# Kernel optimization log

Measured on AMD Instinct MI355X. Metric: run time of the kernel, lower is better.

Reference implementation:

```python
import jax, jax.numpy as jnp
import numpy as np
import math

D = 2048      # hidden_size
H = 16        # num_heads
DH = 128      # head_dim
RQ = 1024     # q_rank
RK = 512      # kv_rank
B, T = 2, 2048

def setup_inputs() -> dict:
    key = jax.random.key(0)
    ks = jax.random.split(key, 8)
    s = lambda fan_in: 1.0 / math.sqrt(fan_in)
    return {
        "x": jax.random.normal(ks[0], (B, T, D), dtype=jnp.float32),
        "Wq_down": jax.random.normal(ks[1], (RQ, D), dtype=jnp.float32) * s(D),
        "Wkv_down": jax.random.normal(ks[2], (RK, D), dtype=jnp.float32) * s(D),
        "Wq_up": jax.random.normal(ks[3], (D, RQ), dtype=jnp.float32) * s(RQ),
        "Wk_up": jax.random.normal(ks[4], (D, RK), dtype=jnp.float32) * s(RK),
        "Wv_up": jax.random.normal(ks[5], (D, RK), dtype=jnp.float32) * s(RK),
        "Wo": jax.random.normal(ks[6], (D, D), dtype=jnp.float32) * s(D),
        "bo": jnp.zeros((D,), dtype=jnp.float32),
    }

def _heads_view(w, rank):
    # w: [H*DH, rank] -> [H, rank, DH]  (matches torch view(H,DH,r).transpose(1,2))
    return w.reshape(H, DH, rank).transpose(0, 2, 1)

def reference(x, Wq_down, Wkv_down, Wq_up, Wk_up, Wv_up, Wo, bo):
    Bx, Tx, d = x.shape
    # low-rank down-projections (torch Linear: x @ W.T)
    Q_lat = x @ Wq_down.T            # [B,T,RQ]
    C_kv = x @ Wkv_down.T            # [B,S,RK]  (S == T, no cache)
    S = C_kv.shape[1]
    # absorbed score matrix M = Uq Uk^T / sqrt(d_h): [H,RQ,RK]
    Uq_h = _heads_view(Wq_up, RQ)    # [H,RQ,DH]
    Uk_h = _heads_view(Wk_up, RK)    # [H,RK,DH]
    Mmat = jnp.einsum('hqd,hkd->hqk', Uq_h, Uk_h) * (1.0 / math.sqrt(DH))
    # logits in latent space: [B,H,T,S]
    logits = jnp.einsum('btq,hqk,bsk->bhts', Q_lat, Mmat, C_kv)
    # causal mask (P = S - T = 0)
    P = S - Tx
    i = jnp.arange(Tx)[:, None]
    j = jnp.arange(S)[None, :]
    neg_inf = jnp.float32(-jnp.inf)
    logits = jnp.where((j > P + i)[None, None], neg_inf, logits)
    # fp32 softmax (every causal row has >=1 valid key, no NaNs)
    attn = jax.nn.softmax(logits.astype(jnp.float32), axis=-1).astype(x.dtype)
    # value up-projection per head: [B,H,S,DH]
    Uv_h = _heads_view(Wv_up, RK)    # [H,RK,DH]
    V_up = jnp.einsum('bsr,hrd->bhsd', C_kv, Uv_h)
    ctx = jnp.einsum('bhts,bhsd->bhtd', attn, V_up)      # [B,H,T,DH]
    ctx = ctx.transpose(0, 2, 1, 3).reshape(Bx, Tx, H * DH)
    out = ctx @ Wo.T + bo
    return out
```

## Files before the change

kernel.cpp:

```cpp
#include <hip/hip_runtime.h>

typedef __bf16 bf16x8 __attribute__((ext_vector_type(8)));
typedef float f32x4 __attribute__((ext_vector_type(4)));
typedef float f32x16 __attribute__((ext_vector_type(16)));
typedef unsigned short u16x4 __attribute__((ext_vector_type(4)));
typedef unsigned int u32x4 __attribute__((ext_vector_type(4)));

#define L2E 1.44269504088896340736f

__device__ __forceinline__ f32x4 mfma16(bf16x8 a, bf16x8 b, f32x4 c) {
  return __builtin_amdgcn_mfma_f32_16x16x32_bf16(a, b, c, 0, 0, 0);
}
__device__ __forceinline__ f32x16 mfma32(bf16x8 a, bf16x8 b, f32x16 c) {
  return __builtin_amdgcn_mfma_f32_32x32x16_bf16(a, b, c, 0, 0, 0);
}

__device__ __forceinline__ void async16(const __bf16* g, __bf16* l) {
  __builtin_amdgcn_global_load_lds(
      (const __attribute__((address_space(1))) void*)g,
      (__attribute__((address_space(3))) void*)l, 16, 0, 0);
}

__device__ __forceinline__ unsigned pk(float x, float y) {
  unsigned short lo = __builtin_bit_cast(unsigned short, (__bf16)x);
  unsigned short hi = __builtin_bit_cast(unsigned short, (__bf16)y);
  return ((unsigned)hi << 16) | (unsigned)lo;
}

__global__ __launch_bounds__(256) void cvt_bf16(const float* __restrict__ s,
                                                __bf16* __restrict__ d) {
  long i = (long)(blockIdx.x * 256 + threadIdx.x) * 4;
  f32x4 v = *(const f32x4*)(s + i);
  u16x4 o;
#pragma unroll
  for (int j = 0; j < 4; j++) o[j] = __builtin_bit_cast(unsigned short, (__bf16)v[j]);
  *(u16x4*)((unsigned short*)d + i) = o;
}

__global__ __launch_bounds__(256) void cvt_w(
    const float* __restrict__ wqd, const float* __restrict__ wkvd,
    const float* __restrict__ wqup, const float* __restrict__ wkup,
    const float* __restrict__ wvup, __bf16* __restrict__ dqkv,
    __bf16* __restrict__ dqu, __bf16* __restrict__ dku,
    __bf16* __restrict__ dvu) {
  int bx = blockIdx.x;
  const float* s;
  __bf16* d;
  int off;
  if (bx < 2048)      { s = wqd;  d = dqkv;                off = bx; }
  else if (bx < 3072) { s = wkvd; d = dqkv + 1024 * 2048;  off = bx - 2048; }
  else if (bx < 5120) { s = wqup; d = dqu;                 off = bx - 3072; }
  else if (bx < 6144) { s = wkup; d = dku;                 off = bx - 5120; }
  else                { s = wvup; d = dvu;                 off = bx - 6144; }
  long i = (long)off * 1024 + threadIdx.x * 4;
  f32x4 v = *(const f32x4*)(s + i);
  u16x4 o;
#pragma unroll
  for (int j = 0; j < 4; j++) o[j] = __builtin_bit_cast(unsigned short, (__bf16)v[j]);
  *(u16x4*)((unsigned short*)d + i) = o;
}

template <int OUTF32>
__device__ __forceinline__ void gemm_body(
    __bf16* As, __bf16* Bs, const __bf16* __restrict__ A,
    const __bf16* __restrict__ Bt, void* __restrict__ Cout,
    const float* __restrict__ bias, int lda, int ldb, int ldc, int N, int K,
    float scale, int bx, int by, int permn) {
  const int tid = threadIdx.x;
  const int wid = tid >> 6, lane = tid & 63;
  const int lrow = lane & 15, lkhi = lane >> 4;
  const int row0 = bx * 128, col0 = by * 128;
  const int wr = (wid >> 1) * 64, wc = (wid & 1) * 64;

  const int trow = tid >> 2;
  const int scol = 8 * ((tid & 3) ^ (trow & 3));
  const __bf16* pA0 = A + (size_t)(row0 + trow) * lda + scol;
  const __bf16* pA1 = pA0 + (size_t)64 * lda;
  const __bf16* pB0 = Bt + (size_t)(col0 + trow) * ldb + scol;
  const __bf16* pB1 = pB0 + (size_t)64 * ldb;
  __bf16* lA0 = As + wid * 512;
  __bf16* lA1 = As + 2048 + wid * 512;
  __bf16* lB0 = Bs + wid * 512;
  __bf16* lB1 = Bs + 2048 + wid * 512;

  int aoff[4], boff[4];
#pragma unroll
  for (int i = 0; i < 4; i++) {
    int rr = wr + i * 16 + lrow;
    aoff[i] = rr * 32 + 8 * (lkhi ^ (rr & 3));
    rr = wc + i * 16 + lrow;
    boff[i] = rr * 32 + 8 * (lkhi ^ (rr & 3));
  }

  f32x4 acc[4][4] = {};
  for (int k0 = 0; k0 < K; k0 += 32) {
    __syncthreads();
    async16(pA0, lA0);
    async16(pA1, lA1);
    async16(pB0, lB0);
    async16(pB1, lB1);
    pA0 += 32; pA1 += 32; pB0 += 32; pB1 += 32;
    __syncthreads();
    bf16x8 af[4], bv[4];
#pragma unroll
    for (int mi = 0; mi < 4; mi++) af[mi] = *(const bf16x8*)(As + aoff[mi]);
#pragma unroll
    for (int ni = 0; ni < 4; ni++) bv[ni] = *(const bf16x8*)(Bs + boff[ni]);
#pragma unroll
    for (int mi = 0; mi < 4; mi++)
#pragma unroll
      for (int ni = 0; ni < 4; ni++)
        acc[mi][ni] = mfma16(af[mi], bv[ni], acc[mi][ni]);
  }

  const int orow = row0 + wr + lkhi * 4;
  const int prow = permn ? ((lrow & 3) | ((lrow & 4) << 1) | ((lrow & 8) >> 1))
                         : lrow;
  const int ocol = col0 + wc + prow;
#pragma unroll
  for (int mi = 0; mi < 4; mi++)
#pragma unroll
    for (int ni = 0; ni < 4; ni++)
#pragma unroll
      for (int r = 0; r < 4; r++) {
        size_t idx = (size_t)(orow + mi * 16 + r) * ldc + (ocol + ni * 16);
        float v = acc[mi][ni][r] * scale;
        if (OUTF32)
          ((float*)Cout)[idx] = v + bias[ocol + ni * 16];
        else
          ((__bf16*)Cout)[idx] = (__bf16)v;
      }
}

template <int OUTF32, int PERMN = 0>
__global__ __launch_bounds__(256, 3) void gemm_bt(
    const __bf16* __restrict__ A, const __bf16* __restrict__ Bt,
    void* __restrict__ Cout, const float* __restrict__ bias,
    int lda, int ldb, int ldc, int N, int K, float scale) {
  __shared__ __align__(16) __bf16 As[4096];
  __shared__ __align__(16) __bf16 Bs[4096];
  gemm_body<OUTF32>(As, Bs, A, Bt, Cout, bias, lda, ldb, ldc, N, K, scale,
                    blockIdx.x, blockIdx.y, PERMN);
}

__global__ __launch_bounds__(256, 3) void gemm_mid(
    const __bf16* __restrict__ qlat, const __bf16* __restrict__ ckv,
    const __bf16* __restrict__ wqu, const __bf16* __restrict__ wku,
    const __bf16* __restrict__ wvu, __bf16* __restrict__ qf,
    __bf16* __restrict__ kf, __bf16* __restrict__ vt) {
  __shared__ __align__(16) __bf16 As[4096];
  __shared__ __align__(16) __bf16 Bs[4096];
  int bid = (int)blockIdx.x;
  if (bid < 512) {
    gemm_body<0>(As, Bs, qlat, wqu, qf, nullptr, 1536, 1024, 2048, 2048, 1024,
                 0.12752039360437355f, bid & 31, bid >> 5, 0);
  } else if (bid < 1024) {
    bid -= 512;
    gemm_body<0>(As, Bs, ckv, wku, kf, nullptr, 1536, 512, 2048, 2048, 512,
                 1.0f, bid & 31, bid >> 5, 0);
  } else {
    bid -= 1024;
    gemm_body<0>(As, Bs, wvu, ckv, vt, nullptr, 512, 1536, 4096, 4096, 512,
                 1.0f, bid & 15, bid >> 4, 1);
  }
}

__global__ __launch_bounds__(256, 2) void mla_attn(
    const __bf16* __restrict__ Qf, const __bf16* __restrict__ Kf,
    const __bf16* __restrict__ Vt, __bf16* __restrict__ ctx) {
  __shared__ __align__(16) __bf16 Ks[2][64 * 128];
  __shared__ __align__(16) __bf16 Vs[2][128 * 64];

  const int r_ = (int)blockIdx.x;
  const int qt = (r_ < 256) ? (15 - (r_ >> 5)) : ((r_ - 256) >> 5);
  const int bh = r_ & 31;
  const int h = bh >> 1, b = bh & 1;
  const int tid = threadIdx.x, wid = tid >> 6, lane = tid & 63;
  const int l31 = lane & 31;
  const bool hh = (lane & 32) != 0;

  const __bf16* Kbh = Kf + (size_t)b * 2048 * 2048 + h * 128;
  const __bf16* Vbh = Vt + (size_t)h * 128 * 4096 + b * 2048;

  auto stage = [&](int k0, int buf) {
#pragma unroll
    for (int i = 0; i < 4; i++) {
      int e = i * 2048 + tid * 8;
      int krow = e >> 7;
      int kcol = (e & 127) ^ (8 * (krow & 15));
      async16(Kbh + (size_t)(k0 + krow) * 2048 + kcol,
              &Ks[buf][i * 2048 + wid * 512]);
    }
#pragma unroll
    for (int i = 0; i < 4; i++) {
      int e = i * 2048 + tid * 8;
      int vrow = e >> 6;
      int vcol = (e & 63) ^ (8 * (vrow & 7));
      async16(Vbh + (size_t)vrow * 4096 + k0 + vcol,
              &Vs[buf][i * 2048 + wid * 512]);
    }
  };

  const int q0 = qt * 128;
  const int nkv = 2 * qt + 2;
  const int q = q0 + wid * 32 + l31;

  bf16x8 qb[8];
  const __bf16* qrow =
      Qf + (size_t)(b * 2048 + q) * 2048 + h * 128 + (hh ? 8 : 0);
#pragma unroll
  for (int ds = 0; ds < 8; ds++) qb[ds] = *(const bf16x8*)(qrow + ds * 16);

  f32x16 o[4] = {};
  float mrow = -1e30f, lsum = 0.f;

  int cur = 0;
  stage(0, 0);

  for (int kb = 0; kb < nkv; kb++) {
    const int k0 = kb * 64;
    __syncthreads();
    if (kb + 1 < nkv) stage(k0 + 64, cur ^ 1);

    f32x16 sa[2] = {}, sb[2] = {};
    __builtin_amdgcn_s_setprio(1);
#pragma unroll
    for (int ds = 0; ds < 4; ds++) {
#pragma unroll
      for (int kt = 0; kt < 2; kt++) {
        int row = kt * 32 + l31;
        int col = (ds * 16 + (hh ? 8 : 0)) ^ (8 * (row & 15));
        bf16x8 kfr = *(const bf16x8*)(&Ks[cur][row * 128 + col]);
        sa[kt] = mfma32(kfr, qb[ds], sa[kt]);
      }
    }
#pragma unroll
    for (int ds = 4; ds < 8; ds++) {
#pragma unroll
      for (int kt = 0; kt < 2; kt++) {
        int row = kt * 32 + l31;
        int col = (ds * 16 + (hh ? 8 : 0)) ^ (8 * (row & 15));
        bf16x8 kfr = *(const bf16x8*)(&Ks[cur][row * 128 + col]);
        sb[kt] = mfma32(kfr, qb[ds], sb[kt]);
      }
    }
    __builtin_amdgcn_s_setprio(0);
    f32x16 sacc[2];
    sacc[0] = sa[0] + sb[0];
    sacc[1] = sa[1] + sb[1];

    if (kb >= 2 * qt) {
#pragma unroll
      for (int kt = 0; kt < 2; kt++)
#pragma unroll
        for (int r = 0; r < 16; r++) {
          int key = k0 + kt * 32 + (r & 3) + 8 * (r >> 2) + (hh ? 4 : 0);
          if (key > q) sacc[kt][r] = -1e30f;
        }
    }

    float t[16];
#pragma unroll
    for (int r = 0; r < 16; r++) t[r] = fmaxf(sacc[0][r], sacc[1][r]);
#pragma unroll
    for (int s = 8; s; s >>= 1)
#pragma unroll
      for (int r = 0; r < s; r++) t[r] = fmaxf(t[r], t[r + s]);
    float pm = fmaxf(t[0], __shfl_xor(t[0], 32));

    if (__any(pm > mrow + 8.f)) {
      float mn = fmaxf(mrow, pm);
      float sf = __builtin_amdgcn_exp2f(mrow - mn);
      mrow = mn;
      lsum *= sf;
#pragma unroll
      for (int r = 0; r < 16; r++) {
        int ql = (r & 3) + 8 * (r >> 2) + (hh ? 4 : 0);
        float sr = __shfl(sf, ql);
#pragma unroll
        for (int dt = 0; dt < 4; dt++) o[dt][r] *= sr;
      }
    }
    float ps0 = 0.f, ps1 = 0.f, ps2 = 0.f, ps3 = 0.f;
#pragma unroll
    for (int kt = 0; kt < 2; kt++)
#pragma unroll
      for (int r = 0; r < 16; r += 4) {
        float a0 = __builtin_amdgcn_exp2f(sacc[kt][r + 0] - mrow);
        float a1 = __builtin_amdgcn_exp2f(sacc[kt][r + 1] - mrow);
        float a2 = __builtin_amdgcn_exp2f(sacc[kt][r + 2] - mrow);
        float a3 = __builtin_amdgcn_exp2f(sacc[kt][r + 3] - mrow);
        sacc[kt][r + 0] = a0; sacc[kt][r + 1] = a1;
        sacc[kt][r + 2] = a2; sacc[kt][r + 3] = a3;
        ps0 += a0; ps1 += a1; ps2 += a2; ps3 += a3;
      }
    float ps = (ps0 + ps1) + (ps2 + ps3);
    ps += __shfl_xor(ps, 32);
    lsum += ps;

    __builtin_amdgcn_s_setprio(1);
#pragma unroll
    for (int s = 0; s < 4; s++) {
      const int kt = s >> 1, r8 = (s & 1) * 8;
      u32x4 wv;
      wv.x = pk(sacc[kt][r8 + 0], sacc[kt][r8 + 1]);
      wv.y = pk(sacc[kt][r8 + 2], sacc[kt][r8 + 3]);
      wv.z = pk(sacc[kt][r8 + 4], sacc[kt][r8 + 5]);
      wv.w = pk(sacc[kt][r8 + 6], sacc[kt][r8 + 7]);
      bf16x8 pa = __builtin_bit_cast(bf16x8, wv);
#pragma unroll
      for (int dt = 0; dt < 4; dt++) {
        int vrow = dt * 32 + l31;
        int vcol = (s * 16 + (hh ? 8 : 0)) ^ (8 * (vrow & 7));
        bf16x8 vf = *(const bf16x8*)(&Vs[cur][vrow * 64 + vcol]);
        o[dt] = mfma32(pa, vf, o[dt]);
      }
    }
    __builtin_amdgcn_s_setprio(0);
    cur ^= 1;
  }

  float inv = 1.f / lsum;
#pragma unroll
  for (int r = 0; r < 16; r++) {
    int ql = (r & 3) + 8 * (r >> 2) + (hh ? 4 : 0);
    float ir = __shfl(inv, ql);
    size_t rowi = (size_t)(b * 2048 + q0 + wid * 32 + ql) * 2048 + h * 128;
#pragma unroll
    for (int dt = 0; dt < 4; dt++)
      ctx[rowi + dt * 32 + l31] = (__bf16)(o[dt][r] * ir);
  }
}

extern "C" void kernel_launch(void* const* d_in, const int* in_sizes, int n_in,
                              void* d_out, int out_size, void* d_ws, size_t ws_size,
                              hipStream_t stream) {
  (void)in_sizes; (void)n_in; (void)out_size; (void)ws_size;
  const float* x    = (const float*)d_in[0];
  const float* wqd  = (const float*)d_in[1];
  const float* wkvd = (const float*)d_in[2];
  const float* wqup = (const float*)d_in[3];
  const float* wkup = (const float*)d_in[4];
  const float* wvup = (const float*)d_in[5];
  const float* wo   = (const float*)d_in[6];
  const float* bo   = (const float*)d_in[7];

  char* ws = (char*)d_ws;
  const size_t MB = 1024 * 1024;
  __bf16* x_bf     = (__bf16*)(ws + 0);
  __bf16* q_full   = (__bf16*)(ws + 16 * MB);
  __bf16* k_full   = (__bf16*)(ws + 32 * MB);
  __bf16* vt       = (__bf16*)(ws + 48 * MB);
  __bf16* qkv_lat  = (__bf16*)(ws + 64 * MB);
  __bf16* wqkvd_bf = (__bf16*)(ws + 76 * MB);
  __bf16* wqup_bf  = (__bf16*)(ws + 82 * MB);
  __bf16* wkup_bf  = (__bf16*)(ws + 86 * MB);
  __bf16* wvup_bf  = (__bf16*)(ws + 88 * MB);
  __bf16* ctx   = x_bf;
  __bf16* wo_bf = qkv_lat;

  cvt_bf16<<<8192, 256, 0, stream>>>(x, x_bf);
  cvt_w<<<7168, 256, 0, stream>>>(wqd, wkvd, wqup, wkup, wvup, wqkvd_bf,
                                  wqup_bf, wkup_bf, wvup_bf);

  dim3 blk(256);
  gemm_bt<0><<<dim3(32, 12), blk, 0, stream>>>(x_bf, wqkvd_bf, qkv_lat, nullptr,
                                               2048, 2048, 1536, 1536, 2048, 1.0f);
  gemm_mid<<<1536, blk, 0, stream>>>(qkv_lat, qkv_lat + 1024, wqup_bf, wkup_bf,
                                     wvup_bf, q_full, k_full, vt);
  cvt_bf16<<<4096, 256, 0, stream>>>(wo, wo_bf);
  mla_attn<<<512, blk, 0, stream>>>(q_full, k_full, vt, ctx);
  gemm_bt<1><<<dim3(32, 16), blk, 0, stream>>>(ctx, wo_bf, (float*)d_out, bo,
                                               2048, 2048, 2048, 2048, 2048, 1.0f);
}
```

Baseline: 226.7 us.

## Split causal KV range across two half-blocks in attention and merge in LDS

The attention kernel now launches 512-thread blocks. Each block splits its query tile's causal key range into two halves, and each half of 256 threads runs its own double-buffered online softmax over its share of the tiles. At the end, the second half writes its partial output and row max/sum to shared memory, and the first half rescales and combines both before writing ctx. This halves the serial per-block loop length to improve load balance across the triangular workload. In exchange, each block uses about 128KB of LDS, which allows only one block per CU, and it adds a merge step with extra syncs.

Measured after the change: 222.0 us. -2.1%, faster.

```diff
diff --git a/kernel.cpp b/kernel.cpp
--- a/kernel.cpp
+++ b/kernel.cpp
@@ -165,45 +165,53 @@
   }
 }
 
-__global__ __launch_bounds__(256, 2) void mla_attn(
+__global__ __launch_bounds__(512, 1) void mla_attn(
     const __bf16* __restrict__ Qf, const __bf16* __restrict__ Kf,
     const __bf16* __restrict__ Vt, __bf16* __restrict__ ctx) {
-  __shared__ __align__(16) __bf16 Ks[2][64 * 128];
-  __shared__ __align__(16) __bf16 Vs[2][128 * 64];
-
-  const int r_ = (int)blockIdx.x;
-  const int qt = (r_ < 256) ? (15 - (r_ >> 5)) : ((r_ - 256) >> 5);
-  const int bh = r_ & 31;
+  __shared__ __align__(16) __bf16 SM[2][32768];
+  __shared__ float MLm[128], MLl[128];
+
+  const int bid = (int)blockIdx.x;
+  const int qt = 15 - (bid >> 5);
+  const int bh = bid & 31;
   const int h = bh >> 1, b = bh & 1;
-  const int tid = threadIdx.x, wid = tid >> 6, lane = tid & 63;
+  const int tid = threadIdx.x;
+  const int half = tid >> 8;
+  const int htid = tid & 255;
+  const int wid4 = htid >> 6;
+  const int lane = tid & 63;
   const int l31 = lane & 31;
   const bool hh = (lane & 32) != 0;
 
+  __bf16* Ks = &SM[half][0];
+  __bf16* Vs = &SM[half][16384];
+
   const __bf16* Kbh = Kf + (size_t)b * 2048 * 2048 + h * 128;
   const __bf16* Vbh = Vt + (size_t)h * 128 * 4096 + b * 2048;
 
   auto stage = [&](int k0, int buf) {
 #pragma unroll
     for (int i = 0; i < 4; i++) {
-      int e = i * 2048 + tid * 8;
+      int e = i * 2048 + htid * 8;
       int krow = e >> 7;
       int kcol = (e & 127) ^ (8 * (krow & 15));
       async16(Kbh + (size_t)(k0 + krow) * 2048 + kcol,
-              &Ks[buf][i * 2048 + wid * 512]);
+              Ks + buf * 8192 + i * 2048 + wid4 * 512);
     }
 #pragma unroll
     for (int i = 0; i < 4; i++) {
-      int e = i * 2048 + tid * 8;
+      int e = i * 2048 + htid * 8;
       int vrow = e >> 6;
       int vcol = (e & 63) ^ (8 * (vrow & 7));
       async16(Vbh + (size_t)vrow * 4096 + k0 + vcol,
-              &Vs[buf][i * 2048 + wid * 512]);
+              Vs + buf * 8192 + i * 2048 + wid4 * 512);
     }
   };
 
   const int q0 = qt * 128;
-  const int nkv = 2 * qt + 2;
-  const int q = q0 + wid * 32 + l31;
+  const int ntile = qt + 1;
+  const int kbase = half * ntile;
+  const int q = q0 + wid4 * 32 + l31;
 
   bf16x8 qb[8];
   const __bf16* qrow =
@@ -215,12 +223,13 @@
   float mrow = -1e30f, lsum = 0.f;
 
   int cur = 0;
-  stage(0, 0);
-
-  for (int kb = 0; kb < nkv; kb++) {
+  stage(kbase * 64, 0);
+
+  for (int t = 0; t < ntile; t++) {
+    const int kb = kbase + t;
     const int k0 = kb * 64;
     __syncthreads();
-    if (kb + 1 < nkv) stage(k0 + 64, cur ^ 1);
+    if (t + 1 < ntile) stage(k0 + 64, cur ^ 1);
 
     f32x16 sa[2] = {}, sb[2] = {};
     __builtin_amdgcn_s_setprio(1);
@@ -230,7 +239,7 @@
       for (int kt = 0; kt < 2; kt++) {
         int row = kt * 32 + l31;
         int col = (ds * 16 + (hh ? 8 : 0)) ^ (8 * (row & 15));
-        bf16x8 kfr = *(const bf16x8*)(&Ks[cur][row * 128 + col]);
+        bf16x8 kfr = *(const bf16x8*)(Ks + cur * 8192 + row * 128 + col);
         sa[kt] = mfma32(kfr, qb[ds], sa[kt]);
       }
     }
@@ -240,7 +249,7 @@
       for (int kt = 0; kt < 2; kt++) {
         int row = kt * 32 + l31;
         int col = (ds * 16 + (hh ? 8 : 0)) ^ (8 * (row & 15));
-        bf16x8 kfr = *(const bf16x8*)(&Ks[cur][row * 128 + col]);
+        bf16x8 kfr = *(const bf16x8*)(Ks + cur * 8192 + row * 128 + col);
         sb[kt] = mfma32(kfr, qb[ds], sb[kt]);
       }
     }
@@ -259,14 +268,14 @@
         }
     }
 
-    float t[16];
-#pragma unroll
-    for (int r = 0; r < 16; r++) t[r] = fmaxf(sacc[0][r], sacc[1][r]);
+    float t16[16];
+#pragma unroll
+    for (int r = 0; r < 16; r++) t16[r] = fmaxf(sacc[0][r], sacc[1][r]);
 #pragma unroll
     for (int s = 8; s; s >>= 1)
 #pragma unroll
-      for (int r = 0; r < s; r++) t[r] = fmaxf(t[r], t[r + s]);
-    float pm = fmaxf(t[0], __shfl_xor(t[0], 32));
+      for (int r = 0; r < s; r++) t16[r] = fmaxf(t16[r], t16[r + s]);
+    float pm = fmaxf(t16[0], __shfl_xor(t16[0], 32));
 
     if (__any(pm > mrow + 8.f)) {
       float mn = fmaxf(mrow, pm);
@@ -312,7 +321,7 @@
       for (int dt = 0; dt < 4; dt++) {
         int vrow = dt * 32 + l31;
         int vcol = (s * 16 + (hh ? 8 : 0)) ^ (8 * (vrow & 7));
-        bf16x8 vf = *(const bf16x8*)(&Vs[cur][vrow * 64 + vcol]);
+        bf16x8 vf = *(const bf16x8*)(Vs + cur * 8192 + vrow * 64 + vcol);
         o[dt] = mfma32(pa, vf, o[dt]);
       }
     }
@@ -320,15 +329,37 @@
     cur ^= 1;
   }
 
-  float inv = 1.f / lsum;
-#pragma unroll
-  for (int r = 0; r < 16; r++) {
-    int ql = (r & 3) + 8 * (r >> 2) + (hh ? 4 : 0);
-    float ir = __shfl(inv, ql);
-    size_t rowi = (size_t)(b * 2048 + q0 + wid * 32 + ql) * 2048 + h * 128;
-#pragma unroll
-    for (int dt = 0; dt < 4; dt++)
-      ctx[rowi + dt * 32 + l31] = (__bf16)(o[dt][r] * ir);
+  __syncthreads();
+  float* om = (float*)&SM[1][0];
+  if (half == 1) {
+#pragma unroll
+    for (int dt = 0; dt < 4; dt++) {
+      int base = ((wid4 * 4 + dt) * 64 + lane) * 16;
+#pragma unroll
+      for (int r = 0; r < 16; r++) om[base + r] = o[dt][r];
+    }
+    if (!hh) { MLm[wid4 * 32 + l31] = mrow; MLl[wid4 * 32 + l31] = lsum; }
+  }
+  __syncthreads();
+  if (half == 0) {
+#pragma unroll
+    for (int r = 0; r < 16; r++) {
+      int ql = (r & 3) + 8 * (r >> 2) + (hh ? 4 : 0);
+      float m0r = __shfl(mrow, ql);
+      float l0r = __shfl(lsum, ql);
+      float m1r = MLm[wid4 * 32 + ql];
+      float l1r = MLl[wid4 * 32 + ql];
+      float M = fmaxf(m0r, m1r);
+      float w0 = __builtin_amdgcn_exp2f(m0r - M);
+      float w1 = __builtin_amdgcn_exp2f(m1r - M);
+      float inv = 1.f / (l0r * w0 + l1r * w1);
+      size_t rowi = (size_t)(b * 2048 + q0 + wid4 * 32 + ql) * 2048 + h * 128;
+#pragma unroll
+      for (int dt = 0; dt < 4; dt++) {
+        float o1v = om[((wid4 * 4 + dt) * 64 + lane) * 16 + r];
+        ctx[rowi + dt * 32 + l31] = (__bf16)((o[dt][r] * w0 + o1v * w1) * inv);
+      }
+    }
   }
 }
 
@@ -369,7 +400,7 @@
   gemm_mid<<<1536, blk, 0, stream>>>(qkv_lat, qkv_lat + 1024, wqup_bf, wkup_bf,
                                      wvup_bf, q_full, k_full, vt);
   cvt_bf16<<<4096, 256, 0, stream>>>(wo, wo_bf);
-  mla_attn<<<512, blk, 0, stream>>>(q_full, k_full, vt, ctx);
+  mla_attn<<<512, 512, 0, stream>>>(q_full, k_full, vt, ctx);
   gemm_bt<1><<<dim3(32, 16), blk, 0, stream>>>(ctx, wo_bf, (float*)d_out, bo,
                                                2048, 2048, 2048, 2048, 2048, 1.0f);
 }
```
